# Performance work log

Hardware: AMD Instinct MI355X
Metric: run time of the kernel (lower is better)

The kernel has to match this reference:

```python
import jax, jax.numpy as jnp
import numpy as np


def logdotexp(A, B):
    # Stable log-domain matmul: logsumexp_k(A[m,k] + B[k,n]) without the 3D broadcast.
    amax = jnp.max(A, axis=1, keepdims=True)   # [m,1]
    bmax = jnp.max(B, axis=0, keepdims=True)   # [1,n]
    return jnp.log(jnp.exp(A - amax) @ jnp.exp(B - bmax)) + amax + bmax


def setup_inputs() -> dict:
    key = jax.random.key(0)
    k1, k2, k3, k4 = jax.random.split(key, 4)
    C, S, N, T = 64, 256, 2000, 500
    return {
        "unnormalized_state_init": jax.random.normal(k1, (C, S), dtype=jnp.float32),
        "unnormalized_chain_weights": jax.random.normal(k2, (T, C), dtype=jnp.float32),
        "unnormalized_emission_matrix": jax.random.normal(k3, (S, N), dtype=jnp.float32),
        "unnormalized_transition_matrix": jax.random.normal(k4, (S, S), dtype=jnp.float32),
        "emissions_mask": jnp.ones((S, N), dtype=jnp.float32),
    }


def reference(unnormalized_state_init, unnormalized_chain_weights,
              unnormalized_emission_matrix, unnormalized_transition_matrix,
              emissions_mask):
    log_state_init = jax.nn.log_softmax(unnormalized_state_init, axis=1)        # [C,S]
    log_chain_weights = jax.nn.log_softmax(unnormalized_chain_weights, axis=1)  # [T,C]
    log_E_ = jax.nn.log_softmax(unnormalized_emission_matrix, axis=1) + jnp.log(emissions_mask)
    log_E = log_E_ - jax.scipy.special.logsumexp(log_E_, axis=1, keepdims=True)  # [S,N]
    log_Tm = jax.nn.log_softmax(unnormalized_transition_matrix, axis=1)          # [S,S]

    T = unnormalized_chain_weights.shape[0]
    C, S = log_state_init.shape
    N = log_E.shape[1]

    def step(h, _):
        h_next = logdotexp(h, log_Tm)  # [C,S]
        return h_next, h_next

    _, hs = jax.lax.scan(step, log_state_init, None, length=T - 1)  # [T-1,C,S]
    log_hidden = jnp.concatenate([log_state_init[None], hs], axis=0)  # [T,C,S]

    # Emission for all timesteps at once via one big stabilized matmul.
    log_obs_ = logdotexp(log_hidden.reshape(T * C, S), log_E).reshape(T, C, N)  # [T,C,N]
    log_obs = jax.scipy.special.logsumexp(log_obs_ + log_chain_weights[:, :, None], axis=1)  # [T,N]
    return log_obs, log_obs_, log_hidden
```

## Files before the change

kernel.cpp:

```cpp
#include <hip/hip_runtime.h>
#include <cstddef>

typedef unsigned short u16;
typedef float f32x4 __attribute__((ext_vector_type(4)));
typedef short bf16x8 __attribute__((ext_vector_type(8)));

#define SDIM 256
#define CDIM 64
#define NDIM 2000
#define TDIM 500

#define MAT  (SDIM*SDIM)
#define HMAT (CDIM*SDIM)

#define OFF_POW    0u
#define OFF_R2     (OFF_POW + 25u*MAT)
#define OFF_R4     (OFF_R2 + MAT)
#define OFF_R8     (OFF_R4 + MAT)
#define OFF_R16    (OFF_R8 + MAT)
#define OFF_HEADS  (OFF_R16 + MAT)
#define OFF_CW     (OFF_HEADS + 20u*HMAT)
#define OFF_EPROB  (OFF_CW + 32000u)
#define OFF_ET     (OFF_EPROB + 512000u)
#define OFF_PT     (OFF_ET + 262144u)
#define OFF_HDB    (OFF_PT + 819200u)
#define OFF_HB     (OFF_HDB + 163840u)

#define OUT_OBSB  1000000u
#define OUT_HIDB  65000000u

#define TP 260

__device__ __forceinline__ float waveMax(float v) {
#pragma unroll
  for (int o = 32; o >= 1; o >>= 1) v = fmaxf(v, __shfl_xor(v, o));
  return v;
}
__device__ __forceinline__ float waveSum(float v) {
#pragma unroll
  for (int o = 32; o >= 1; o >>= 1) v += __shfl_xor(v, o);
  return v;
}
__device__ __forceinline__ u16 f2b(float f) {
  union { float f; unsigned u; } x; x.f = f;
  return (u16)((x.u + 0x7fffu + ((x.u >> 16) & 1u)) >> 16);
}

__global__ __launch_bounds__(256) void prep_prob(
    const float* __restrict__ si, const float* __restrict__ cw,
    const float* __restrict__ em, const float* __restrict__ tm,
    const float* __restrict__ mask, float* __restrict__ ws) {
  int b = blockIdx.x;
  const float* src; const float* msk = nullptr; float* dst; int len;
  if (b < 64)       { src = si + b*SDIM;                 dst = ws + OFF_HEADS + b*SDIM; len = SDIM; }
  else if (b < 564) { int r = b - 64;  src = cw + r*64;  dst = ws + OFF_CW + r*64;      len = 64;   }
  else if (b < 820) { int r = b - 564; src = tm + (size_t)r*SDIM; dst = ws + OFF_POW + (size_t)r*SDIM; len = SDIM; }
  else              { int r = b - 820; src = em + (size_t)r*NDIM; dst = ws + OFF_EPROB + (size_t)r*NDIM; len = NDIM; msk = mask + (size_t)r*NDIM; }
  int tid = threadIdx.x;
  __shared__ float rA[4], rB[4];
  float m = -INFINITY;
  for (int i = tid; i < len; i += 256) {
    float v = src[i];
    if (msk) v += __logf(msk[i]);
    m = fmaxf(m, v);
  }
  m = waveMax(m);
  if ((tid & 63) == 0) rA[tid >> 6] = m;
  __syncthreads();
  m = fmaxf(fmaxf(rA[0], rA[1]), fmaxf(rA[2], rA[3]));
  float s = 0.f;
  for (int i = tid; i < len; i += 256) {
    float v = src[i];
    if (msk) v += __logf(msk[i]);
    s += __expf(v - m);
  }
  s = waveSum(s);
  if ((tid & 63) == 0) rB[tid >> 6] = s;
  __syncthreads();
  s = rB[0] + rB[1] + rB[2] + rB[3];
  float inv = 1.f / s;
  for (int i = tid; i < len; i += 256) {
    float v = src[i];
    if (msk) v += __logf(msk[i]);
    dst[i] = __expf(v - m) * inv;
  }
}

__device__ void gemm_tile(const float* __restrict__ A, const float* __restrict__ B,
                          float* __restrict__ C, int r0, int n0) {
  __shared__ float As[64][68];
  __shared__ float Bs[64][68];
  int tid = threadIdx.x;
  float acc[4][4] = {};
  int tm4 = (tid >> 4) << 2, tn4 = (tid & 15) << 2;
  for (int kc = 0; kc < 4; ++kc) {
    __syncthreads();
    {
      int rr = tid >> 2, p = tid & 3;
      const float* sA = A + (size_t)(r0 + rr)*SDIM + kc*64 + p*16;
#pragma unroll
      for (int i = 0; i < 16; ++i) As[p*16 + i][rr] = sA[i];
    }
    {
      int kk = tid >> 2, p = tid & 3;
      const float* sB = B + (size_t)(kc*64 + kk)*SDIM + n0 + p*16;
#pragma unroll
      for (int i = 0; i < 16; ++i) Bs[kk][p*16 + i] = sB[i];
    }
    __syncthreads();
#pragma unroll 8
    for (int k = 0; k < 64; ++k) {
      float4 av = *(const float4*)&As[k][tm4];
      float4 bv = *(const float4*)&Bs[k][tn4];
      float a[4] = {av.x, av.y, av.z, av.w};
      float bb[4] = {bv.x, bv.y, bv.z, bv.w};
#pragma unroll
      for (int i = 0; i < 4; ++i)
#pragma unroll
        for (int j = 0; j < 4; ++j) acc[i][j] += a[i]*bb[j];
    }
  }
#pragma unroll
  for (int i = 0; i < 4; ++i)
    *(float4*)&C[(size_t)(r0 + tm4 + i)*SDIM + n0 + tn4] =
        make_float4(acc[i][0], acc[i][1], acc[i][2], acc[i][3]);
}

struct Jobs {
  int n;
  unsigned aOff[12], bOff[12], cOff[12];
  int M[12];
};

__global__ __launch_bounds__(256) void gemm_kernel(float* __restrict__ ws, Jobs jobs) {
  int j = blockIdx.z;
  if (blockIdx.x * 64 >= jobs.M[j]) return;
  gemm_tile(ws + jobs.aOff[j], ws + jobs.bOff[j], ws + jobs.cOff[j],
            blockIdx.x * 64, blockIdx.y * 64);
}

__global__ __launch_bounds__(256) void transpose_b16(
    const float* __restrict__ srcBase, int ldn, int nReal, unsigned srcZ,
    u16* __restrict__ dstBase, unsigned dstZ) {
  const float* src = srcBase + (size_t)blockIdx.z * srcZ;
  u16* dst = dstBase + (size_t)blockIdx.z * dstZ;
  int n0 = blockIdx.x * 64, k0 = blockIdx.y * 64;
  __shared__ float tile[64][65];
  int tid = threadIdx.x;
  {
    int kk = tid >> 2, p = tid & 3;
    const float* s = src + (size_t)(k0 + kk)*ldn + n0 + p*16;
#pragma unroll
    for (int i = 0; i < 16; ++i) {
      int n = n0 + p*16 + i;
      tile[p*16 + i][kk] = (n < nReal) ? s[i] : 0.f;
    }
  }
  __syncthreads();
  {
    int rr = tid >> 2, kq = (tid & 3) * 16;
    unsigned w[8];
#pragma unroll
    for (int i = 0; i < 8; ++i)
      w[i] = (unsigned)f2b(tile[rr][kq + 2*i]) | ((unsigned)f2b(tile[rr][kq + 2*i + 1]) << 16);
    uint4* d = (uint4*)(dst + (size_t)(n0 + rr)*256 + k0 + kq);
    d[0] = *(uint4*)&w[0];
    d[1] = *(uint4*)&w[4];
  }
}

__global__ __launch_bounds__(256) void prep_headsb(float* __restrict__ ws_f) {
  int b = blockIdx.x, tid = threadIdx.x;
  const float* src = ws_f + OFF_HEADS + (size_t)b*HMAT;
  u16* dst = (u16*)(ws_f + OFF_HDB) + (size_t)b*HMAT;
  for (int i = tid; i < HMAT/2; i += 256) {
    float2 v = *(const float2*)(src + 2*i);
    ((unsigned*)dst)[i] = (unsigned)f2b(v.x) | ((unsigned)f2b(v.y) << 16);
  }
}

__device__ __forceinline__ void stageAB(int tid, const u16* __restrict__ gA,
                                        const u16* __restrict__ gB, int kc,
                                        char* ldsA, char* ldsB) {
#pragma unroll
  for (int p = 0; p < 2; ++p) {
    int row = p*32 + (tid >> 3), slot = tid & 7;
    uint4 v = *(const uint4*)((const char*)gA + (size_t)row*512 + kc*128 + slot*16);
    *(uint4*)(ldsA + row*128 + ((slot*16) ^ ((row & 7) << 4))) = v;
  }
#pragma unroll
  for (int p = 0; p < 8; ++p) {
    int row = p*32 + (tid >> 3), slot = tid & 7;
    uint4 v = *(const uint4*)((const char*)gB + (size_t)row*512 + kc*128 + slot*16);
    *(uint4*)(ldsB + row*128 + ((slot*16) ^ ((row & 7) << 4))) = v;
  }
}

__device__ __forceinline__ void mfma_block(int g16, int c16, int wid,
                                           const char* ldsA, const char* ldsB,
                                           f32x4 (&acc)[4][4]) {
#pragma unroll
  for (int ks = 0; ks < 2; ++ks) {
    bf16x8 af[4], bfr[4];
    int kb = ks*64 + g16*16;
#pragma unroll
    for (int mf = 0; mf < 4; ++mf) {
      int row = mf*16 + c16;
      af[mf] = *(const bf16x8*)(ldsA + row*128 + (kb ^ ((row & 7) << 4)));
    }
#pragma unroll
    for (int nf = 0; nf < 4; ++nf) {
      int n = wid*64 + nf*16 + c16;
      bfr[nf] = *(const bf16x8*)(ldsB + n*128 + (kb ^ ((n & 7) << 4)));
    }
#pragma unroll
    for (int mf = 0; mf < 4; ++mf)
#pragma unroll
      for (int nf = 0; nf < 4; ++nf)
        acc[mf][nf] = __builtin_amdgcn_mfma_f32_16x16x32_bf16(af[mf], bfr[nf], acc[mf][nf], 0, 0, 0);
  }
}

__global__ __launch_bounds__(256) void fill_mfma(float* __restrict__ ws_f, float* __restrict__ out) {
  int tt = blockIdx.x;
  int b = tt / 25, j = tt % 25;
  int tid = threadIdx.x;
  float* hid = out + OUT_HIDB + (size_t)tt*HMAT;
  u16* hb = (u16*)(ws_f + OFF_HB) + (size_t)tt*HMAT;
  if (j == 0) {
    const float* H = ws_f + OFF_HEADS + (size_t)b*HMAT;
    for (int i = tid; i < HMAT; i += 256) {
      float v = H[i];
      hid[i] = __logf(v);
      hb[i] = f2b(v);
    }
    return;
  }
  const u16* gA = (const u16*)(ws_f + OFF_HDB) + (size_t)b*HMAT;
  const u16* gB = (const u16*)(ws_f + OFF_PT) + (size_t)(j - 1)*MAT;
  __shared__ __align__(16) char smem[41600];
  char* ldsA = smem; char* ldsB = smem + 8192;
  int wid = tid >> 6, lane = tid & 63, g16 = lane >> 4, c16 = lane & 15;
  f32x4 acc[4][4];
#pragma unroll
  for (int mf = 0; mf < 4; ++mf)
#pragma unroll
    for (int nf = 0; nf < 4; ++nf) acc[mf][nf] = {0.f, 0.f, 0.f, 0.f};
  stageAB(tid, gA, gB, 0, ldsA, ldsB);
  __syncthreads();
  for (int kc = 0; kc < 4; ++kc) {
    mfma_block(g16, c16, wid, ldsA, ldsB, acc);
    __syncthreads();
    if (kc < 3) { stageAB(tid, gA, gB, kc + 1, ldsA, ldsB); __syncthreads(); }
  }
  float* tile = (float*)smem;
#pragma unroll
  for (int p = 0; p < 2; ++p) {
    if (p) __syncthreads();
#pragma unroll
    for (int mf = 2*p; mf < 2*p + 2; ++mf)
#pragma unroll
      for (int r = 0; r < 4; ++r) {
        int lrow = mf*16 + g16*4 + r - 32*p;
#pragma unroll
        for (int nf = 0; nf < 4; ++nf) {
          int n = wid*64 + nf*16 + c16;
          tile[lrow*TP + n] = acc[mf][nf][r];
        }
      }
    __syncthreads();
#pragma unroll
    for (int r8 = 0; r8 < 8; ++r8) {
      int row = wid*8 + r8;
      int c = 32*p + row;
      f32x4 v = *(const f32x4*)&tile[row*TP + lane*4];
      f32x4 lg = {__logf(v[0]), __logf(v[1]), __logf(v[2]), __logf(v[3])};
      __builtin_nontemporal_store(lg, (f32x4*)(hid + (size_t)c*256 + lane*4));
      uint2 w;
      w.x = (unsigned)f2b(v[0]) | ((unsigned)f2b(v[1]) << 16);
      w.y = (unsigned)f2b(v[2]) | ((unsigned)f2b(v[3]) << 16);
      *(uint2*)(hb + (size_t)c*256 + lane*4) = w;
    }
  }
}

__global__ __launch_bounds__(256) void emission_mfma(const float* __restrict__ ws_f, float* __restrict__ out) {
  int tt = blockIdx.y, n0 = blockIdx.x * 256;
  int tid = threadIdx.x;
  const u16* gA = (const u16*)(ws_f + OFF_HB) + (size_t)tt*HMAT;
  const u16* gB = (const u16*)(ws_f + OFF_ET) + (size_t)n0*256;
  __shared__ __align__(16) char smem[41600];
  __shared__ float sCw[64];
  char* ldsA = smem; char* ldsB = smem + 8192;
  if (tid < 64) sCw[tid] = ws_f[OFF_CW + tt*64 + tid];
  int wid = tid >> 6, lane = tid & 63, g16 = lane >> 4, c16 = lane & 15;
  f32x4 acc[4][4];
#pragma unroll
  for (int mf = 0; mf < 4; ++mf)
#pragma unroll
    for (int nf = 0; nf < 4; ++nf) acc[mf][nf] = {0.f, 0.f, 0.f, 0.f};
  stageAB(tid, gA, gB, 0, ldsA, ldsB);
  __syncthreads();
  for (int kc = 0; kc < 4; ++kc) {
    mfma_block(g16, c16, wid, ldsA, ldsB, acc);
    __syncthreads();
    if (kc < 3) { stageAB(tid, gA, gB, kc + 1, ldsA, ldsB); __syncthreads(); }
  }
  float s[4] = {0.f, 0.f, 0.f, 0.f};
  int nn[4];
#pragma unroll
  for (int nf = 0; nf < 4; ++nf) nn[nf] = n0 + wid*64 + nf*16 + c16;
#pragma unroll
  for (int mf = 0; mf < 4; ++mf)
#pragma unroll
    for (int r = 0; r < 4; ++r) {
      float wc = sCw[mf*16 + g16*4 + r];
#pragma unroll
      for (int nf = 0; nf < 4; ++nf) s[nf] += acc[mf][nf][r] * wc;
    }
#pragma unroll
  for (int nf = 0; nf < 4; ++nf) {
    s[nf] += __shfl_xor(s[nf], 16);
    s[nf] += __shfl_xor(s[nf], 32);
  }
  if (g16 == 0) {
#pragma unroll
    for (int nf = 0; nf < 4; ++nf)
      if (nn[nf] < NDIM) out[(size_t)tt*NDIM + nn[nf]] = __logf(s[nf]);
  }
  float* obsb = out + OUT_OBSB + (size_t)tt*CDIM*NDIM;
  float* tile = (float*)smem;
  bool okc = (n0 + (lane + 1)*4 <= NDIM);
#pragma unroll
  for (int p = 0; p < 2; ++p) {
    __syncthreads();
#pragma unroll
    for (int mf = 2*p; mf < 2*p + 2; ++mf)
#pragma unroll
      for (int r = 0; r < 4; ++r) {
        int lrow = mf*16 + g16*4 + r - 32*p;
#pragma unroll
        for (int nf = 0; nf < 4; ++nf) {
          int n = wid*64 + nf*16 + c16;
          tile[lrow*TP + n] = acc[mf][nf][r];
        }
      }
    __syncthreads();
#pragma unroll
    for (int r8 = 0; r8 < 8; ++r8) {
      int row = wid*8 + r8;
      int c = 32*p + row;
      if (okc) {
        f32x4 v = *(const f32x4*)&tile[row*TP + lane*4];
        f32x4 lg = {__logf(v[0]), __logf(v[1]), __logf(v[2]), __logf(v[3])};
        __builtin_nontemporal_store(lg, (f32x4*)(obsb + (size_t)c*NDIM + n0 + lane*4));
      }
    }
  }
}

extern "C" void kernel_launch(void* const* d_in, const int* in_sizes, int n_in,
                              void* d_out, int out_size, void* d_ws, size_t ws_size,
                              hipStream_t stream) {
  const float* si   = (const float*)d_in[0];
  const float* cw   = (const float*)d_in[1];
  const float* em   = (const float*)d_in[2];
  const float* tm   = (const float*)d_in[3];
  const float* mask = (const float*)d_in[4];
  float* out = (float*)d_out;
  float* ws  = (float*)d_ws;
  dim3 blk(256);

  prep_prob<<<dim3(1076), blk, 0, stream>>>(si, cw, em, tm, mask, ws);

  transpose_b16<<<dim3(32, 4, 1), blk, 0, stream>>>(ws + OFF_EPROB, NDIM, NDIM, 0,
                                                    (u16*)(ws + OFF_ET), 0);

  auto powOff  = [](int j){ return (unsigned)(OFF_POW + (unsigned)j*MAT); };
  auto headOff = [](int b){ return (unsigned)(OFF_HEADS + (unsigned)b*HMAT); };
  Jobs s;

  s.n = 1; s.aOff[0]=powOff(0); s.bOff[0]=powOff(0); s.cOff[0]=powOff(1); s.M[0]=256;
  gemm_kernel<<<dim3(4,4,1), blk, 0, stream>>>(ws, s);
  s.n = 2;
  s.aOff[0]=powOff(1); s.bOff[0]=powOff(0); s.cOff[0]=powOff(2); s.M[0]=256;
  s.aOff[1]=powOff(1); s.bOff[1]=powOff(1); s.cOff[1]=powOff(3); s.M[1]=256;
  gemm_kernel<<<dim3(4,4,2), blk, 0, stream>>>(ws, s);
  s.n = 4;
  for (int i=0;i<4;++i){ s.aOff[i]=powOff(3); s.bOff[i]=powOff(i); s.cOff[i]=powOff(4+i); s.M[i]=256; }
  gemm_kernel<<<dim3(4,4,4), blk, 0, stream>>>(ws, s);
  s.n = 8;
  for (int i=0;i<8;++i){ s.aOff[i]=powOff(7); s.bOff[i]=powOff(i); s.cOff[i]=powOff(8+i); s.M[i]=256; }
  gemm_kernel<<<dim3(4,4,8), blk, 0, stream>>>(ws, s);
  s.n = 9;
  for (int i=0;i<9;++i){ s.aOff[i]=powOff(15); s.bOff[i]=powOff(i); s.cOff[i]=powOff(16+i); s.M[i]=256; }
  gemm_kernel<<<dim3(4,4,9), blk, 0, stream>>>(ws, s);

  transpose_b16<<<dim3(4, 4, 25), blk, 0, stream>>>(ws + OFF_POW, SDIM, SDIM, MAT,
                                                    (u16*)(ws + OFF_PT), MAT);

  s.n = 2;
  s.aOff[0]=headOff(0); s.bOff[0]=powOff(24); s.cOff[0]=headOff(1); s.M[0]=64;
  s.aOff[1]=powOff(24); s.bOff[1]=powOff(24); s.cOff[1]=OFF_R2;     s.M[1]=256;
  gemm_kernel<<<dim3(4,4,2), blk, 0, stream>>>(ws, s);
  s.n = 3;
  s.aOff[0]=headOff(0); s.bOff[0]=OFF_R2; s.cOff[0]=headOff(2); s.M[0]=64;
  s.aOff[1]=headOff(1); s.bOff[1]=OFF_R2; s.cOff[1]=headOff(3); s.M[1]=64;
  s.aOff[2]=OFF_R2;     s.bOff[2]=OFF_R2; s.cOff[2]=OFF_R4;     s.M[2]=256;
  gemm_kernel<<<dim3(4,4,3), blk, 0, stream>>>(ws, s);
  s.n = 5;
  for (int i=0;i<4;++i){ s.aOff[i]=headOff(i); s.bOff[i]=OFF_R4; s.cOff[i]=headOff(4+i); s.M[i]=64; }
  s.aOff[4]=OFF_R4; s.bOff[4]=OFF_R4; s.cOff[4]=OFF_R8; s.M[4]=256;
  gemm_kernel<<<dim3(4,4,5), blk, 0, stream>>>(ws, s);
  s.n = 9;
  for (int i=0;i<8;++i){ s.aOff[i]=headOff(i); s.bOff[i]=OFF_R8; s.cOff[i]=headOff(8+i); s.M[i]=64; }
  s.aOff[8]=OFF_R8; s.bOff[8]=OFF_R8; s.cOff[8]=OFF_R16; s.M[8]=256;
  gemm_kernel<<<dim3(4,4,9), blk, 0, stream>>>(ws, s);
  s.n = 4;
  for (int i=0;i<4;++i){ s.aOff[i]=headOff(i); s.bOff[i]=OFF_R16; s.cOff[i]=headOff(16+i); s.M[i]=64; }
  gemm_kernel<<<dim3(4,4,4), blk, 0, stream>>>(ws, s);

  prep_headsb<<<dim3(20), blk, 0, stream>>>(ws);

  fill_mfma<<<dim3(500), blk, 0, stream>>>(ws, out);

  emission_mfma<<<dim3(8,500), blk, 0, stream>>>(ws, out);
}
```

Baseline: 490.7 us.

## Fuse prep, matrix-power chain and transposes into one persistent grid-synced kernel

Replaces the sequence of about fourteen small launches (softmax prep, staged GEMMs for transition-matrix powers and head propagation, bf16 transposes, head conversion) with one persistent kernel of 256 blocks. The stages are separated by atomic-counter grid barriers, and the transposes are folded into otherwise idle stages. This removes per-launch overhead and tail idle time on a chain of tiny, latency-bound GEMMs. In exchange it needs a memset of the counter each call, relies on all 256 blocks being co-resident so the spin barrier cannot deadlock, and adds barrier latency. The prep row softmax now keeps values in registers instead of reloading them three times.

```diff
diff --git a/kernel.cpp b/kernel.cpp
--- a/kernel.cpp
+++ b/kernel.cpp
@@ -12,6 +12,8 @@
 
 #define MAT  (SDIM*SDIM)
 #define HMAT (CDIM*SDIM)
+
+#define GRID 256
 
 #define OFF_POW    0u
 #define OFF_R2     (OFF_POW + 25u*MAT)
@@ -25,6 +27,7 @@
 #define OFF_PT     (OFF_ET + 262144u)
 #define OFF_HDB    (OFF_PT + 819200u)
 #define OFF_HB     (OFF_HDB + 163840u)
+#define OFF_CNT    (OFF_HB + 4096000u)
 
 #define OUT_OBSB  1000000u
 #define OUT_HIDB  65000000u
@@ -46,50 +49,63 @@
   return (u16)((x.u + 0x7fffu + ((x.u >> 16) & 1u)) >> 16);
 }
 
-__global__ __launch_bounds__(256) void prep_prob(
+__device__ __forceinline__ void grid_sync(unsigned* cnt, unsigned target) {
+  __syncthreads();
+  if (threadIdx.x == 0) {
+    __threadfence();
+    atomicAdd(cnt, 1u);
+    while (atomicOr(cnt, 0u) < target) __builtin_amdgcn_s_sleep(8);
+    __threadfence();
+  }
+  __syncthreads();
+}
+
+__device__ __forceinline__ void prep_row(int b,
     const float* __restrict__ si, const float* __restrict__ cw,
     const float* __restrict__ em, const float* __restrict__ tm,
-    const float* __restrict__ mask, float* __restrict__ ws) {
-  int b = blockIdx.x;
+    const float* __restrict__ mask, float* __restrict__ ws,
+    float* rA, float* rB) {
   const float* src; const float* msk = nullptr; float* dst; int len;
   if (b < 64)       { src = si + b*SDIM;                 dst = ws + OFF_HEADS + b*SDIM; len = SDIM; }
   else if (b < 564) { int r = b - 64;  src = cw + r*64;  dst = ws + OFF_CW + r*64;      len = 64;   }
   else if (b < 820) { int r = b - 564; src = tm + (size_t)r*SDIM; dst = ws + OFF_POW + (size_t)r*SDIM; len = SDIM; }
   else              { int r = b - 820; src = em + (size_t)r*NDIM; dst = ws + OFF_EPROB + (size_t)r*NDIM; len = NDIM; msk = mask + (size_t)r*NDIM; }
   int tid = threadIdx.x;
-  __shared__ float rA[4], rB[4];
+  __syncthreads();
+  float v[8];
   float m = -INFINITY;
-  for (int i = tid; i < len; i += 256) {
-    float v = src[i];
-    if (msk) v += __logf(msk[i]);
-    m = fmaxf(m, v);
+#pragma unroll
+  for (int i = 0; i < 8; ++i) {
+    int idx = tid + i*256;
+    if (idx < len) {
+      float x = src[idx];
+      if (msk) x += __logf(msk[idx]);
+      v[i] = x;
+      m = fmaxf(m, x);
+    } else v[i] = -INFINITY;
   }
   m = waveMax(m);
   if ((tid & 63) == 0) rA[tid >> 6] = m;
   __syncthreads();
   m = fmaxf(fmaxf(rA[0], rA[1]), fmaxf(rA[2], rA[3]));
   float s = 0.f;
-  for (int i = tid; i < len; i += 256) {
-    float v = src[i];
-    if (msk) v += __logf(msk[i]);
-    s += __expf(v - m);
-  }
+#pragma unroll
+  for (int i = 0; i < 8; ++i) s += __expf(v[i] - m);
   s = waveSum(s);
   if ((tid & 63) == 0) rB[tid >> 6] = s;
   __syncthreads();
   s = rB[0] + rB[1] + rB[2] + rB[3];
   float inv = 1.f / s;
-  for (int i = tid; i < len; i += 256) {
-    float v = src[i];
-    if (msk) v += __logf(msk[i]);
-    dst[i] = __expf(v - m) * inv;
+#pragma unroll
+  for (int i = 0; i < 8; ++i) {
+    int idx = tid + i*256;
+    if (idx < len) dst[idx] = __expf(v[i] - m) * inv;
   }
 }
 
 __device__ void gemm_tile(const float* __restrict__ A, const float* __restrict__ B,
-                          float* __restrict__ C, int r0, int n0) {
-  __shared__ float As[64][68];
-  __shared__ float Bs[64][68];
+                          float* __restrict__ C, int r0, int n0,
+                          float (*As)[68], float (*Bs)[68]) {
   int tid = threadIdx.x;
   float acc[4][4] = {};
   int tm4 = (tid >> 4) << 2, tn4 = (tid & 15) << 2;
@@ -120,33 +136,18 @@
         for (int j = 0; j < 4; ++j) acc[i][j] += a[i]*bb[j];
     }
   }
+  __syncthreads();
 #pragma unroll
   for (int i = 0; i < 4; ++i)
     *(float4*)&C[(size_t)(r0 + tm4 + i)*SDIM + n0 + tn4] =
         make_float4(acc[i][0], acc[i][1], acc[i][2], acc[i][3]);
 }
 
-struct Jobs {
-  int n;
-  unsigned aOff[12], bOff[12], cOff[12];
-  int M[12];
-};
-
-__global__ __launch_bounds__(256) void gemm_kernel(float* __restrict__ ws, Jobs jobs) {
-  int j = blockIdx.z;
-  if (blockIdx.x * 64 >= jobs.M[j]) return;
-  gemm_tile(ws + jobs.aOff[j], ws + jobs.bOff[j], ws + jobs.cOff[j],
-            blockIdx.x * 64, blockIdx.y * 64);
-}
-
-__global__ __launch_bounds__(256) void transpose_b16(
-    const float* __restrict__ srcBase, int ldn, int nReal, unsigned srcZ,
-    u16* __restrict__ dstBase, unsigned dstZ) {
-  const float* src = srcBase + (size_t)blockIdx.z * srcZ;
-  u16* dst = dstBase + (size_t)blockIdx.z * dstZ;
-  int n0 = blockIdx.x * 64, k0 = blockIdx.y * 64;
-  __shared__ float tile[64][65];
-  int tid = threadIdx.x;
+__device__ void trans_tile(const float* __restrict__ src, int ldn, int nReal,
+                           u16* __restrict__ dst, int n0, int k0,
+                           float (*tile)[65]) {
+  int tid = threadIdx.x;
+  __syncthreads();
   {
     int kk = tid >> 2, p = tid & 3;
     const float* s = src + (size_t)(k0 + kk)*ldn + n0 + p*16;
@@ -169,13 +170,62 @@
   }
 }
 
-__global__ __launch_bounds__(256) void prep_headsb(float* __restrict__ ws_f) {
-  int b = blockIdx.x, tid = threadIdx.x;
-  const float* src = ws_f + OFF_HEADS + (size_t)b*HMAT;
-  u16* dst = (u16*)(ws_f + OFF_HDB) + (size_t)b*HMAT;
-  for (int i = tid; i < HMAT/2; i += 256) {
-    float2 v = *(const float2*)(src + 2*i);
-    ((unsigned*)dst)[i] = (unsigned)f2b(v.x) | ((unsigned)f2b(v.y) << 16);
+struct MJobs {
+  unsigned a[47], b[47], c[47];
+  unsigned short tiles[47];
+  unsigned char start[10], cnt[10];
+  unsigned short stTiles[10];
+};
+
+__global__ __launch_bounds__(256) void mega_chain(
+    const float* __restrict__ si, const float* __restrict__ cw,
+    const float* __restrict__ em, const float* __restrict__ tm,
+    const float* __restrict__ mask, float* __restrict__ ws, MJobs jb) {
+  __shared__ float As[64][68];
+  __shared__ float Bs[64][68];
+  __shared__ float tile[64][65];
+  __shared__ float rA[4], rB[4];
+  unsigned* cnt = (unsigned*)(ws + OFF_CNT);
+  int bid = blockIdx.x;
+
+  for (int r = bid; r < 1076; r += GRID)
+    prep_row(r, si, cw, em, tm, mask, ws, rA, rB);
+  grid_sync(cnt, GRID);
+
+  for (int s = 0; s < 10; ++s) {
+    int mt = jb.stTiles[s];
+    int extra = (s == 0) ? 128 : (s == 5 ? 400 : 0);
+    for (int j = bid; j < mt + extra; j += GRID) {
+      if (j < mt) {
+        int t = j, k = jb.start[s];
+        while (t >= jb.tiles[k]) { t -= jb.tiles[k]; ++k; }
+        int r0, n0;
+        if (jb.tiles[k] == 16) { r0 = (t >> 2) << 6; n0 = (t & 3) << 6; }
+        else { r0 = 0; n0 = t << 6; }
+        gemm_tile(ws + jb.a[k], ws + jb.b[k], ws + jb.c[k], r0, n0, As, Bs);
+      } else if (s == 0) {
+        int e = j - mt;
+        trans_tile(ws + OFF_EPROB, NDIM, NDIM, (u16*)(ws + OFF_ET),
+                   (e >> 2) * 64, (e & 3) * 64, tile);
+      } else {
+        int e = j - mt;
+        int m = e >> 4, t = e & 15;
+        trans_tile(ws + OFF_POW + (size_t)m*MAT, SDIM, SDIM,
+                   (u16*)(ws + OFF_PT) + (size_t)m*MAT,
+                   (t >> 2) * 64, (t & 3) * 64, tile);
+      }
+    }
+    grid_sync(cnt, GRID * (s + 2));
+  }
+
+  int tid = threadIdx.x;
+  for (int j = bid; j < 20; j += GRID) {
+    const float* src = ws + OFF_HEADS + (size_t)j*HMAT;
+    u16* dst = (u16*)(ws + OFF_HDB) + (size_t)j*HMAT;
+    for (int i = tid; i < HMAT/2; i += 256) {
+      float2 v = *(const float2*)(src + 2*i);
+      ((unsigned*)dst)[i] = (unsigned)f2b(v.x) | ((unsigned)f2b(v.y) << 16);
+    }
   }
 }
 
@@ -371,58 +421,41 @@
   float* ws  = (float*)d_ws;
   dim3 blk(256);
 
-  prep_prob<<<dim3(1076), blk, 0, stream>>>(si, cw, em, tm, mask, ws);
-
-  transpose_b16<<<dim3(32, 4, 1), blk, 0, stream>>>(ws + OFF_EPROB, NDIM, NDIM, 0,
-                                                    (u16*)(ws + OFF_ET), 0);
-
+  MJobs jb;
+  int ji = 0;
   auto powOff  = [](int j){ return (unsigned)(OFF_POW + (unsigned)j*MAT); };
   auto headOff = [](int b){ return (unsigned)(OFF_HEADS + (unsigned)b*HMAT); };
-  Jobs s;
-
-  s.n = 1; s.aOff[0]=powOff(0); s.bOff[0]=powOff(0); s.cOff[0]=powOff(1); s.M[0]=256;
-  gemm_kernel<<<dim3(4,4,1), blk, 0, stream>>>(ws, s);
-  s.n = 2;
-  s.aOff[0]=powOff(1); s.bOff[0]=powOff(0); s.cOff[0]=powOff(2); s.M[0]=256;
-  s.aOff[1]=powOff(1); s.bOff[1]=powOff(1); s.cOff[1]=powOff(3); s.M[1]=256;
-  gemm_kernel<<<dim3(4,4,2), blk, 0, stream>>>(ws, s);
-  s.n = 4;
-  for (int i=0;i<4;++i){ s.aOff[i]=powOff(3); s.bOff[i]=powOff(i); s.cOff[i]=powOff(4+i); s.M[i]=256; }
-  gemm_kernel<<<dim3(4,4,4), blk, 0, stream>>>(ws, s);
-  s.n = 8;
-  for (int i=0;i<8;++i){ s.aOff[i]=powOff(7); s.bOff[i]=powOff(i); s.cOff[i]=powOff(8+i); s.M[i]=256; }
-  gemm_kernel<<<dim3(4,4,8), blk, 0, stream>>>(ws, s);
-  s.n = 9;
-  for (int i=0;i<9;++i){ s.aOff[i]=powOff(15); s.bOff[i]=powOff(i); s.cOff[i]=powOff(16+i); s.M[i]=256; }
-  gemm_kernel<<<dim3(4,4,9), blk, 0, stream>>>(ws, s);
-
-  transpose_b16<<<dim3(4, 4, 25), blk, 0, stream>>>(ws + OFF_POW, SDIM, SDIM, MAT,
-                                                    (u16*)(ws + OFF_PT), MAT);
-
-  s.n = 2;
-  s.aOff[0]=headOff(0); s.bOff[0]=powOff(24); s.cOff[0]=headOff(1); s.M[0]=64;
-  s.aOff[1]=powOff(24); s.bOff[1]=powOff(24); s.cOff[1]=OFF_R2;     s.M[1]=256;
-  gemm_kernel<<<dim3(4,4,2), blk, 0, stream>>>(ws, s);
-  s.n = 3;
-  s.aOff[0]=headOff(0); s.bOff[0]=OFF_R2; s.cOff[0]=headOff(2); s.M[0]=64;
-  s.aOff[1]=headOff(1); s.bOff[1]=OFF_R2; s.cOff[1]=headOff(3); s.M[1]=64;
-  s.aOff[2]=OFF_R2;     s.bOff[2]=OFF_R2; s.cOff[2]=OFF_R4;     s.M[2]=256;
-  gemm_kernel<<<dim3(4,4,3), blk, 0, stream>>>(ws, s);
-  s.n = 5;
-  for (int i=0;i<4;++i){ s.aOff[i]=headOff(i); s.bOff[i]=OFF_R4; s.cOff[i]=headOff(4+i); s.M[i]=64; }
-  s.aOff[4]=OFF_R4; s.bOff[4]=OFF_R4; s.cOff[4]=OFF_R8; s.M[4]=256;
-  gemm_kernel<<<dim3(4,4,5), blk, 0, stream>>>(ws, s);
-  s.n = 9;
-  for (int i=0;i<8;++i){ s.aOff[i]=headOff(i); s.bOff[i]=OFF_R8; s.cOff[i]=headOff(8+i); s.M[i]=64; }
-  s.aOff[8]=OFF_R8; s.bOff[8]=OFF_R8; s.cOff[8]=OFF_R16; s.M[8]=256;
-  gemm_kernel<<<dim3(4,4,9), blk, 0, stream>>>(ws, s);
-  s.n = 4;
-  for (int i=0;i<4;++i){ s.aOff[i]=headOff(i); s.bOff[i]=OFF_R16; s.cOff[i]=headOff(16+i); s.M[i]=64; }
-  gemm_kernel<<<dim3(4,4,4), blk, 0, stream>>>(ws, s);
-
-  prep_headsb<<<dim3(20), blk, 0, stream>>>(ws);
+  auto addJob = [&](unsigned a, unsigned b, unsigned c, int M) {
+    jb.a[ji] = a; jb.b[ji] = b; jb.c[ji] = c; jb.tiles[ji] = (M == 256) ? 16 : 4; ++ji;
+  };
+  auto stage = [&](int s, int first) {
+    jb.start[s] = (unsigned char)first; jb.cnt[s] = (unsigned char)(ji - first);
+    int t = 0; for (int k = first; k < ji; ++k) t += jb.tiles[k];
+    jb.stTiles[s] = (unsigned short)t;
+  };
+  int f;
+  f = ji; addJob(powOff(0), powOff(0), powOff(1), 256); stage(0, f);
+  f = ji; addJob(powOff(1), powOff(0), powOff(2), 256);
+          addJob(powOff(1), powOff(1), powOff(3), 256); stage(1, f);
+  f = ji; for (int i = 0; i < 4; ++i) addJob(powOff(3), powOff(i), powOff(4+i), 256); stage(2, f);
+  f = ji; for (int i = 0; i < 8; ++i) addJob(powOff(7), powOff(i), powOff(8+i), 256); stage(3, f);
+  f = ji; for (int i = 0; i < 9; ++i) addJob(powOff(15), powOff(i), powOff(16+i), 256); stage(4, f);
+  f = ji; addJob(headOff(0), powOff(24), headOff(1), 64);
+          addJob(powOff(24), powOff(24), OFF_R2, 256); stage(5, f);
+  f = ji; addJob(headOff(0), OFF_R2, headOff(2), 64);
+          addJob(headOff(1), OFF_R2, headOff(3), 64);
+          addJob(OFF_R2, OFF_R2, OFF_R4, 256); stage(6, f);
+  f = ji; for (int i = 0; i < 4; ++i) addJob(headOff(i), OFF_R4, headOff(4+i), 64);
+          addJob(OFF_R4, OFF_R4, OFF_R8, 256); stage(7, f);
+  f = ji; for (int i = 0; i < 8; ++i) addJob(headOff(i), OFF_R8, headOff(8+i), 64);
+          addJob(OFF_R8, OFF_R8, OFF_R16, 256); stage(8, f);
+  f = ji; for (int i = 0; i < 4; ++i) addJob(headOff(i), OFF_R16, headOff(16+i), 64); stage(9, f);
+
+  hipMemsetAsync(ws + OFF_CNT, 0, sizeof(unsigned), stream);
+
+  mega_chain<<<dim3(GRID), blk, 0, stream>>>(si, cw, em, tm, mask, ws, jb);
 
   fill_mfma<<<dim3(500), blk, 0, stream>>>(ws, out);
 
-  emission_mfma<<<dim3(8,500), blk, 0, stream>>>(ws, out);
-}
+  emission_mfma<<<dim3(8, 500), blk, 0, stream>>>(ws, out);
+}
```

New measurement: 655.9 us. 33.7% more time.

## Move power-chain GEMMs to bf16 MFMA with fused transposed outputs

Applied to the files above, without the earlier changes.

Replaces the fp32 SIMT gemm_kernel used to build transition-matrix powers and chain heads with a bf16 MFMA kernel. Each job writes both a row-major bf16 copy and a transposed bf16 copy, which removes the separate transpose and head-conversion passes. The earlier transpose and bf16 prep steps are merged into one prep2 launch. Intermediate powers are now rounded to bf16 at every squaring step, so rounding error can build up along the chain and affect accuracy.

```diff
diff --git a/kernel.cpp b/kernel.cpp
--- a/kernel.cpp
+++ b/kernel.cpp
@@ -14,17 +14,18 @@
 #define HMAT (CDIM*SDIM)
 
 #define OFF_POW    0u
-#define OFF_R2     (OFF_POW + 25u*MAT)
-#define OFF_R4     (OFF_R2 + MAT)
-#define OFF_R8     (OFF_R4 + MAT)
-#define OFF_R16    (OFF_R8 + MAT)
-#define OFF_HEADS  (OFF_R16 + MAT)
-#define OFF_CW     (OFF_HEADS + 20u*HMAT)
+#define OFF_HEADS  (OFF_POW + MAT)
+#define OFF_CW     (OFF_HEADS + HMAT)
 #define OFF_EPROB  (OFF_CW + 32000u)
 #define OFF_ET     (OFF_EPROB + 512000u)
 #define OFF_PT     (OFF_ET + 262144u)
-#define OFF_HDB    (OFF_PT + 819200u)
+#define OFF_PPB    (OFF_PT + 819200u)
+#define OFF_RPB    (OFF_PPB + 819200u)
+#define OFF_RPT    (OFF_RPB + 131072u)
+#define OFF_HDB    (OFF_RPT + 131072u)
 #define OFF_HB     (OFF_HDB + 163840u)
+
+#define U16OFF(X) ((unsigned)((X) * 2u))
 
 #define OUT_OBSB  1000000u
 #define OUT_HIDB  65000000u
@@ -44,6 +45,10 @@
 __device__ __forceinline__ u16 f2b(float f) {
   union { float f; unsigned u; } x; x.f = f;
   return (u16)((x.u + 0x7fffu + ((x.u >> 16) & 1u)) >> 16);
+}
+__device__ __forceinline__ float b2f(u16 b) {
+  union { unsigned u; float f; } x; x.u = ((unsigned)b) << 16;
+  return x.f;
 }
 
 __global__ __launch_bounds__(256) void prep_prob(
@@ -86,66 +91,9 @@
   }
 }
 
-__device__ void gemm_tile(const float* __restrict__ A, const float* __restrict__ B,
-                          float* __restrict__ C, int r0, int n0) {
-  __shared__ float As[64][68];
-  __shared__ float Bs[64][68];
-  int tid = threadIdx.x;
-  float acc[4][4] = {};
-  int tm4 = (tid >> 4) << 2, tn4 = (tid & 15) << 2;
-  for (int kc = 0; kc < 4; ++kc) {
-    __syncthreads();
-    {
-      int rr = tid >> 2, p = tid & 3;
-      const float* sA = A + (size_t)(r0 + rr)*SDIM + kc*64 + p*16;
-#pragma unroll
-      for (int i = 0; i < 16; ++i) As[p*16 + i][rr] = sA[i];
-    }
-    {
-      int kk = tid >> 2, p = tid & 3;
-      const float* sB = B + (size_t)(kc*64 + kk)*SDIM + n0 + p*16;
-#pragma unroll
-      for (int i = 0; i < 16; ++i) Bs[kk][p*16 + i] = sB[i];
-    }
-    __syncthreads();
-#pragma unroll 8
-    for (int k = 0; k < 64; ++k) {
-      float4 av = *(const float4*)&As[k][tm4];
-      float4 bv = *(const float4*)&Bs[k][tn4];
-      float a[4] = {av.x, av.y, av.z, av.w};
-      float bb[4] = {bv.x, bv.y, bv.z, bv.w};
-#pragma unroll
-      for (int i = 0; i < 4; ++i)
-#pragma unroll
-        for (int j = 0; j < 4; ++j) acc[i][j] += a[i]*bb[j];
-    }
-  }
-#pragma unroll
-  for (int i = 0; i < 4; ++i)
-    *(float4*)&C[(size_t)(r0 + tm4 + i)*SDIM + n0 + tn4] =
-        make_float4(acc[i][0], acc[i][1], acc[i][2], acc[i][3]);
-}
-
-struct Jobs {
-  int n;
-  unsigned aOff[12], bOff[12], cOff[12];
-  int M[12];
-};
-
-__global__ __launch_bounds__(256) void gemm_kernel(float* __restrict__ ws, Jobs jobs) {
-  int j = blockIdx.z;
-  if (blockIdx.x * 64 >= jobs.M[j]) return;
-  gemm_tile(ws + jobs.aOff[j], ws + jobs.bOff[j], ws + jobs.cOff[j],
-            blockIdx.x * 64, blockIdx.y * 64);
-}
-
-__global__ __launch_bounds__(256) void transpose_b16(
-    const float* __restrict__ srcBase, int ldn, int nReal, unsigned srcZ,
-    u16* __restrict__ dstBase, unsigned dstZ) {
-  const float* src = srcBase + (size_t)blockIdx.z * srcZ;
-  u16* dst = dstBase + (size_t)blockIdx.z * dstZ;
-  int n0 = blockIdx.x * 64, k0 = blockIdx.y * 64;
-  __shared__ float tile[64][65];
+__device__ void trans_tile(const float* __restrict__ src, int ldn, int nReal,
+                           u16* __restrict__ dst, int n0, int k0,
+                           float (*tile)[65]) {
   int tid = threadIdx.x;
   {
     int kk = tid >> 2, p = tid & 3;
@@ -169,13 +117,30 @@
   }
 }
 
-__global__ __launch_bounds__(256) void prep_headsb(float* __restrict__ ws_f) {
+__global__ __launch_bounds__(256) void prep2(float* __restrict__ ws) {
+  __shared__ float tile[64][65];
   int b = blockIdx.x, tid = threadIdx.x;
-  const float* src = ws_f + OFF_HEADS + (size_t)b*HMAT;
-  u16* dst = (u16*)(ws_f + OFF_HDB) + (size_t)b*HMAT;
-  for (int i = tid; i < HMAT/2; i += 256) {
-    float2 v = *(const float2*)(src + 2*i);
-    ((unsigned*)dst)[i] = (unsigned)f2b(v.x) | ((unsigned)f2b(v.y) << 16);
+  if (b < 128) {
+    trans_tile(ws + OFF_EPROB, NDIM, NDIM, (u16*)ws + U16OFF(OFF_ET), (b >> 2)*64, (b & 3)*64, tile);
+  } else if (b < 144) {
+    int t = b - 128;
+    trans_tile(ws + OFF_POW, SDIM, SDIM, (u16*)ws + U16OFF(OFF_PT), (t >> 2)*64, (t & 3)*64, tile);
+  } else if (b < 152) {
+    int t = b - 144;
+    const float* s = ws + OFF_POW + t*8192;
+    unsigned* d = (unsigned*)((u16*)ws + U16OFF(OFF_PPB)) + t*4096;
+    for (int i = tid; i < 4096; i += 256) {
+      float2 v = *(const float2*)(s + 2*i);
+      d[i] = (unsigned)f2b(v.x) | ((unsigned)f2b(v.y) << 16);
+    }
+  } else {
+    int t = b - 152;
+    const float* s = ws + OFF_HEADS + t*8192;
+    unsigned* d = (unsigned*)((u16*)ws + U16OFF(OFF_HDB)) + t*4096;
+    for (int i = tid; i < 4096; i += 256) {
+      float2 v = *(const float2*)(s + 2*i);
+      d[i] = (unsigned)f2b(v.x) | ((unsigned)f2b(v.y) << 16);
+    }
   }
 }
 
@@ -218,6 +183,82 @@
 #pragma unroll
       for (int nf = 0; nf < 4; ++nf)
         acc[mf][nf] = __builtin_amdgcn_mfma_f32_16x16x32_bf16(af[mf], bfr[nf], acc[mf][nf], 0, 0, 0);
+  }
+}
+
+struct CJobs {
+  int n;
+  unsigned a[12], b[12], cp[12], ct[12];
+  unsigned short tiles[12];
+};
+
+__global__ __launch_bounds__(256) void chain_mfma(float* __restrict__ ws, CJobs jb) {
+  int t = blockIdx.x, k = 0;
+  while (t >= jb.tiles[k]) { t -= jb.tiles[k]; ++k; }
+  int r0 = t * 64;
+  u16* wsu = (u16*)ws;
+  const u16* gA = wsu + jb.a[k] + (size_t)r0*256;
+  const u16* gB = wsu + jb.b[k];
+  u16* cp = wsu + jb.cp[k] + (size_t)r0*256;
+  bool hasCT = (jb.ct[k] != 0xFFFFFFFFu);
+  u16* ctB = wsu + (hasCT ? jb.ct[k] : 0u);
+  int tid = threadIdx.x;
+  __shared__ __align__(16) char smem[41600];
+  char* ldsA = smem; char* ldsB = smem + 8192;
+  int wid = tid >> 6, lane = tid & 63, g16 = lane >> 4, c16 = lane & 15;
+  f32x4 acc[4][4];
+#pragma unroll
+  for (int mf = 0; mf < 4; ++mf)
+#pragma unroll
+    for (int nf = 0; nf < 4; ++nf) acc[mf][nf] = {0.f, 0.f, 0.f, 0.f};
+  stageAB(tid, gA, gB, 0, ldsA, ldsB);
+  __syncthreads();
+  for (int kc = 0; kc < 4; ++kc) {
+    mfma_block(g16, c16, wid, ldsA, ldsB, acc);
+    __syncthreads();
+    if (kc < 3) { stageAB(tid, gA, gB, kc + 1, ldsA, ldsB); __syncthreads(); }
+  }
+  float* tile = (float*)smem;
+#pragma unroll
+  for (int p = 0; p < 2; ++p) {
+    if (p) __syncthreads();
+#pragma unroll
+    for (int mf = 2*p; mf < 2*p + 2; ++mf)
+#pragma unroll
+      for (int r = 0; r < 4; ++r) {
+        int lrow = mf*16 + g16*4 + r - 32*p;
+#pragma unroll
+        for (int nf = 0; nf < 4; ++nf) {
+          int n = wid*64 + nf*16 + c16;
+          tile[lrow*TP + n] = acc[mf][nf][r];
+        }
+      }
+    __syncthreads();
+#pragma unroll
+    for (int r8 = 0; r8 < 8; ++r8) {
+      int row = wid*8 + r8;
+      int m = 32*p + row;
+      f32x4 v = *(const f32x4*)&tile[row*TP + lane*4];
+      uint2 w;
+      w.x = (unsigned)f2b(v[0]) | ((unsigned)f2b(v[1]) << 16);
+      w.y = (unsigned)f2b(v[2]) | ((unsigned)f2b(v[3]) << 16);
+      *(uint2*)(cp + (size_t)m*256 + lane*4) = w;
+    }
+    if (hasCT) {
+#pragma unroll
+      for (int it = 0; it < 4; ++it) {
+        int n = it*64 + lane;
+        unsigned w[16];
+#pragma unroll
+        for (int j = 0; j < 16; ++j)
+          w[j] = (unsigned)f2b(tile[2*j*TP + n]) | ((unsigned)f2b(tile[(2*j+1)*TP + n]) << 16);
+        uint4* d = (uint4*)(ctB + (size_t)n*256 + r0 + 32*p);
+        d[0] = *(uint4*)&w[0];
+        d[1] = *(uint4*)&w[4];
+        d[2] = *(uint4*)&w[8];
+        d[3] = *(uint4*)&w[12];
+      }
+    }
   }
 }
 
@@ -226,18 +267,17 @@
   int b = tt / 25, j = tt % 25;
   int tid = threadIdx.x;
   float* hid = out + OUT_HIDB + (size_t)tt*HMAT;
-  u16* hb = (u16*)(ws_f + OFF_HB) + (size_t)tt*HMAT;
+  u16* hb = (u16*)ws_f + U16OFF(OFF_HB) + (size_t)tt*HMAT;
+  const u16* gA = (u16*)ws_f + U16OFF(OFF_HDB) + (size_t)b*HMAT;
   if (j == 0) {
-    const float* H = ws_f + OFF_HEADS + (size_t)b*HMAT;
     for (int i = tid; i < HMAT; i += 256) {
-      float v = H[i];
-      hid[i] = __logf(v);
-      hb[i] = f2b(v);
+      u16 hv = gA[i];
+      hid[i] = __logf(b2f(hv));
+      hb[i] = hv;
     }
     return;
   }
-  const u16* gA = (const u16*)(ws_f + OFF_HDB) + (size_t)b*HMAT;
-  const u16* gB = (const u16*)(ws_f + OFF_PT) + (size_t)(j - 1)*MAT;
+  const u16* gB = (u16*)ws_f + U16OFF(OFF_PT) + (size_t)(j - 1)*MAT;
   __shared__ __align__(16) char smem[41600];
   char* ldsA = smem; char* ldsB = smem + 8192;
   int wid = tid >> 6, lane = tid & 63, g16 = lane >> 4, c16 = lane & 15;
@@ -287,8 +327,8 @@
 __global__ __launch_bounds__(256) void emission_mfma(const float* __restrict__ ws_f, float* __restrict__ out) {
   int tt = blockIdx.y, n0 = blockIdx.x * 256;
   int tid = threadIdx.x;
-  const u16* gA = (const u16*)(ws_f + OFF_HB) + (size_t)tt*HMAT;
-  const u16* gB = (const u16*)(ws_f + OFF_ET) + (size_t)n0*256;
+  const u16* gA = (const u16*)ws_f + U16OFF(OFF_HB) + (size_t)tt*HMAT;
+  const u16* gB = (const u16*)ws_f + U16OFF(OFF_ET) + (size_t)n0*256;
   __shared__ __align__(16) char smem[41600];
   __shared__ float sCw[64];
   char* ldsA = smem; char* ldsB = smem + 8192;
@@ -372,57 +412,46 @@
   dim3 blk(256);
 
   prep_prob<<<dim3(1076), blk, 0, stream>>>(si, cw, em, tm, mask, ws);
-
-  transpose_b16<<<dim3(32, 4, 1), blk, 0, stream>>>(ws + OFF_EPROB, NDIM, NDIM, 0,
-                                                    (u16*)(ws + OFF_ET), 0);
-
-  auto powOff  = [](int j){ return (unsigned)(OFF_POW + (unsigned)j*MAT); };
-  auto headOff = [](int b){ return (unsigned)(OFF_HEADS + (unsigned)b*HMAT); };
-  Jobs s;
-
-  s.n = 1; s.aOff[0]=powOff(0); s.bOff[0]=powOff(0); s.cOff[0]=powOff(1); s.M[0]=256;
-  gemm_kernel<<<dim3(4,4,1), blk, 0, stream>>>(ws, s);
-  s.n = 2;
-  s.aOff[0]=powOff(1); s.bOff[0]=powOff(0); s.cOff[0]=powOff(2); s.M[0]=256;
-  s.aOff[1]=powOff(1); s.bOff[1]=powOff(1); s.cOff[1]=powOff(3); s.M[1]=256;
-  gemm_kernel<<<dim3(4,4,2), blk, 0, stream>>>(ws, s);
-  s.n = 4;
-  for (int i=0;i<4;++i){ s.aOff[i]=powOff(3); s.bOff[i]=powOff(i); s.cOff[i]=powOff(4+i); s.M[i]=256; }
-  gemm_kernel<<<dim3(4,4,4), blk, 0, stream>>>(ws, s);
-  s.n = 8;
-  for (int i=0;i<8;++i){ s.aOff[i]=powOff(7); s.bOff[i]=powOff(i); s.cOff[i]=powOff(8+i); s.M[i]=256; }
-  gemm_kernel<<<dim3(4,4,8), blk, 0, stream>>>(ws, s);
-  s.n = 9;
-  for (int i=0;i<9;++i){ s.aOff[i]=powOff(15); s.bOff[i]=powOff(i); s.cOff[i]=powOff(16+i); s.M[i]=256; }
-  gemm_kernel<<<dim3(4,4,9), blk, 0, stream>>>(ws, s);
-
-  transpose_b16<<<dim3(4, 4, 25), blk, 0, stream>>>(ws + OFF_POW, SDIM, SDIM, MAT,
-                                                    (u16*)(ws + OFF_PT), MAT);
-
-  s.n = 2;
-  s.aOff[0]=headOff(0); s.bOff[0]=powOff(24); s.cOff[0]=headOff(1); s.M[0]=64;
-  s.aOff[1]=powOff(24); s.bOff[1]=powOff(24); s.cOff[1]=OFF_R2;     s.M[1]=256;
-  gemm_kernel<<<dim3(4,4,2), blk, 0, stream>>>(ws, s);
-  s.n = 3;
-  s.aOff[0]=headOff(0); s.bOff[0]=OFF_R2; s.cOff[0]=headOff(2); s.M[0]=64;
-  s.aOff[1]=headOff(1); s.bOff[1]=OFF_R2; s.cOff[1]=headOff(3); s.M[1]=64;
-  s.aOff[2]=OFF_R2;     s.bOff[2]=OFF_R2; s.cOff[2]=OFF_R4;     s.M[2]=256;
-  gemm_kernel<<<dim3(4,4,3), blk, 0, stream>>>(ws, s);
-  s.n = 5;
-  for (int i=0;i<4;++i){ s.aOff[i]=headOff(i); s.bOff[i]=OFF_R4; s.cOff[i]=headOff(4+i); s.M[i]=64; }
-  s.aOff[4]=OFF_R4; s.bOff[4]=OFF_R4; s.cOff[4]=OFF_R8; s.M[4]=256;
-  gemm_kernel<<<dim3(4,4,5), blk, 0, stream>>>(ws, s);
-  s.n = 9;
-  for (int i=0;i<8;++i){ s.aOff[i]=headOff(i); s.bOff[i]=OFF_R8; s.cOff[i]=headOff(8+i); s.M[i]=64; }
-  s.aOff[8]=OFF_R8; s.bOff[8]=OFF_R8; s.cOff[8]=OFF_R16; s.M[8]=256;
-  gemm_kernel<<<dim3(4,4,9), blk, 0, stream>>>(ws, s);
-  s.n = 4;
-  for (int i=0;i<4;++i){ s.aOff[i]=headOff(i); s.bOff[i]=OFF_R16; s.cOff[i]=headOff(16+i); s.M[i]=64; }
-  gemm_kernel<<<dim3(4,4,4), blk, 0, stream>>>(ws, s);
-
-  prep_headsb<<<dim3(20), blk, 0, stream>>>(ws);
+  prep2<<<dim3(154), blk, 0, stream>>>(ws);
+
+  auto ppb = [](int i){ return U16OFF(OFF_PPB) + (unsigned)i*MAT; };
+  auto pt  = [](int i){ return U16OFF(OFF_PT)  + (unsigned)i*MAT; };
+  auto rpb = [](int i){ return U16OFF(OFF_RPB) + (unsigned)i*MAT; };
+  auto rpt = [](int i){ return U16OFF(OFF_RPT) + (unsigned)i*MAT; };
+  auto hdb = [](int b){ return U16OFF(OFF_HDB) + (unsigned)b*HMAT; };
+
+  CJobs jb;
+  int ji = 0, total = 0;
+  auto add = [&](unsigned a, unsigned b, unsigned cp, unsigned ct, int M) {
+    jb.a[ji] = a; jb.b[ji] = b; jb.cp[ji] = cp; jb.ct[ji] = ct;
+    jb.tiles[ji] = (M == 256) ? 4 : 1; total += jb.tiles[ji]; ++ji;
+  };
+  auto launch = [&]() {
+    jb.n = ji;
+    chain_mfma<<<dim3(total), blk, 0, stream>>>(ws, jb);
+    ji = 0; total = 0;
+  };
+  const unsigned NOCT = 0xFFFFFFFFu;
+
+  add(ppb(0), pt(0), ppb(1), pt(1), 256); launch();
+  add(ppb(1), pt(0), ppb(2), pt(2), 256);
+  add(ppb(1), pt(1), ppb(3), pt(3), 256); launch();
+  for (int i = 0; i < 4; ++i) add(ppb(3), pt(i), ppb(4+i), pt(4+i), 256); launch();
+  for (int i = 0; i < 8; ++i) add(ppb(7), pt(i), ppb(8+i), pt(8+i), 256); launch();
+  for (int i = 0; i < 9; ++i) add(ppb(15), pt(i), ppb(16+i), pt(16+i), 256); launch();
+
+  add(hdb(0), pt(24), hdb(1), NOCT, 64);
+  add(ppb(24), pt(24), rpb(0), rpt(0), 256); launch();
+  add(hdb(0), rpt(0), hdb(2), NOCT, 64);
+  add(hdb(1), rpt(0), hdb(3), NOCT, 64);
+  add(rpb(0), rpt(0), rpb(1), rpt(1), 256); launch();
+  for (int i = 0; i < 4; ++i) add(hdb(i), rpt(1), hdb(4+i), NOCT, 64);
+  add(rpb(1), rpt(1), rpb(2), rpt(2), 256); launch();
+  for (int i = 0; i < 8; ++i) add(hdb(i), rpt(2), hdb(8+i), NOCT, 64);
+  add(rpb(2), rpt(2), rpb(3), rpt(3), 256); launch();
+  for (int i = 0; i < 4; ++i) add(hdb(i), rpt(3), hdb(16+i), NOCT, 64); launch();
 
   fill_mfma<<<dim3(500), blk, 0, stream>>>(ws, out);
 
-  emission_mfma<<<dim3(8,500), blk, 0, stream>>>(ws, out);
-}
+  emission_mfma<<<dim3(8, 500), blk, 0, stream>>>(ws, out);
+}
```

New measurement: 478.5 us. 2.5% less time.
